# Performance work log

Hardware: AMD Instinct MI355X
Metric: run time of the kernel (lower is better)

## Reference

```python
import jax, jax.numpy as jnp
import numpy as np

INPUT_DIM = 1024
NUM_HEADS = 16
HEAD_DIM = INPUT_DIM // NUM_HEADS


def setup_inputs() -> dict:
    key = jax.random.key(0)
    ks = jax.random.split(key, 9)
    d = INPUT_DIM
    s = 1.0 / np.sqrt(d)
    x = jax.random.normal(ks[0], (2, 2048, d), dtype=jnp.float32)
    # nn.Linear default init ~ U(-1/sqrt(in), 1/sqrt(in)); weights stored as (out, in), we keep (in, out)
    Wq = jax.random.uniform(ks[1], (d, d), jnp.float32, -s, s)
    bq = jax.random.uniform(ks[2], (d,), jnp.float32, -s, s)
    Wk = jax.random.uniform(ks[3], (d, d), jnp.float32, -s, s)
    bk = jax.random.uniform(ks[4], (d,), jnp.float32, -s, s)
    Wv = jax.random.uniform(ks[5], (d, d), jnp.float32, -s, s)
    bv = jax.random.uniform(ks[6], (d,), jnp.float32, -s, s)
    Wo = jax.random.uniform(ks[7], (d, d), jnp.float32, -s, s)
    bo = jax.random.uniform(ks[8], (d,), jnp.float32, -s, s)
    return {"x": x, "Wq": Wq, "bq": bq, "Wk": Wk, "bk": bk, "Wv": Wv, "bv": bv, "Wo": Wo, "bo": bo}


def reference(x, Wq, bq, Wk, bk, Wv, bv, Wo, bo):
    b, t, d = x.shape
    h, hd = NUM_HEADS, HEAD_DIM
    # projections -> [b, h, t, hd]
    q = (x @ Wq + bq).reshape(b, t, h, hd).transpose(0, 2, 1, 3)
    k = (x @ Wk + bk).reshape(b, t, h, hd).transpose(0, 2, 1, 3)
    v = (x @ Wv + bv).reshape(b, t, h, hd).transpose(0, 2, 1, 3)
    scores = jnp.einsum('bhqd,bhkd->bhqk', q, k) / jnp.sqrt(jnp.float32(hd))
    probs = jax.nn.softmax(scores, axis=-1)
    out = jnp.einsum('bhqk,bhkd->bhqd', probs, v)
    out = out.transpose(0, 2, 1, 3).reshape(b, t, d)
    return out @ Wo + bo
```

## Files before the change

### kernel.cpp

```cpp
#include <hip/hip_runtime.h>
#include <math.h>


#define BATCH 2
#define SEQ   2048
#define DIM   1024
#define NHEAD 16
#define HDIM  64
#define MROWS (BATCH * SEQ)
#define BH    (BATCH * NHEAD)
#define NKT   (SEQ / 64)

typedef __attribute__((ext_vector_type(4))) float     floatx4;
typedef __attribute__((ext_vector_type(4))) float     float4v;
typedef __attribute__((ext_vector_type(8))) _Float16  half8;
typedef __attribute__((ext_vector_type(4))) _Float16  half4;
typedef __attribute__((ext_vector_type(2))) __fp16    fp16x2;
typedef __attribute__((ext_vector_type(4))) unsigned  uint4v;

#define SOFT_C 5.77078016f
#define QSCALE 0.18033688f

#if __has_builtin(__builtin_amdgcn_exp2f)
#define EXP2F(x) __builtin_amdgcn_exp2f(x)
#else
#define EXP2F(x) exp2f(x)
#endif

__device__ __forceinline__ void gload16(const void* g, void* l) {
    __builtin_amdgcn_global_load_lds(
        (const __attribute__((address_space(1))) unsigned int*)g,
        (__attribute__((address_space(3))) unsigned int*)l, 16, 0, 0);
}

__device__ __forceinline__ unsigned pk2(float a, float b) {
    fp16x2 v = __builtin_amdgcn_cvt_pkrtz(a, b);
    return __builtin_bit_cast(unsigned, v);
}

__device__ __forceinline__ void plswap(unsigned &a, unsigned &b) {
#if __has_builtin(__builtin_amdgcn_permlane32_swap) && __has_builtin(__builtin_amdgcn_permlane16_swap)
    auto r32 = __builtin_amdgcn_permlane32_swap(a, b, false, false);
    auto r16 = __builtin_amdgcn_permlane16_swap(r32[0], r32[1], false, false);
    a = r16[0]; b = r16[1];
#else
    asm volatile("s_nop 1\n\t"
                 "v_permlane32_swap_b32 %0, %1\n\t"
                 "s_nop 1\n\t"
                 "v_permlane16_swap_b32 %0, %1\n\t"
                 "s_nop 1"
                 : "+v"(a), "+v"(b));
#endif
}

__global__ __launch_bounds__(256) void prep(
    const float* __restrict__ x,
    const float* __restrict__ Wq, const float* __restrict__ Wk,
    const float* __restrict__ Wv, const float* __restrict__ Wo,
    _Float16* __restrict__ xh,
    _Float16* __restrict__ Wqt, _Float16* __restrict__ Wkt,
    _Float16* __restrict__ Wvt, _Float16* __restrict__ Wot)
{
    const int tid = threadIdx.x;
    if (blockIdx.z == 4) {
        const int bid = blockIdx.y * 16 + blockIdx.x;
        #pragma unroll
        for (int it = 0; it < 8; ++it) {
            const size_t i = (((size_t)it * 256 + bid) * 256 + tid) * 8;
            float4v a = *(const float4v*)(x + i);
            float4v b = *(const float4v*)(x + i + 4);
            half8 o;
            #pragma unroll
            for (int c = 0; c < 4; ++c) { o[c] = (_Float16)a[c]; o[4+c] = (_Float16)b[c]; }
            *(half8*)(xh + i) = o;
        }
        return;
    }
    __shared__ float tile[64][65];
    const float* W; _Float16* o;
    switch (blockIdx.z) {
        case 0: W = Wq; o = Wqt; break;
        case 1: W = Wk; o = Wkt; break;
        case 2: W = Wv; o = Wvt; break;
        default: W = Wo; o = Wot; break;
    }
    const int n0 = blockIdx.x * 64, k0 = blockIdx.y * 64;
    #pragma unroll
    for (int p = 0; p < 16; ++p) {
        int idx = tid + p * 256;
        int r = idx >> 6, c = idx & 63;
        tile[r][c] = W[(size_t)(k0 + r) * DIM + n0 + c];
    }
    __syncthreads();
    #pragma unroll
    for (int p = 0; p < 16; ++p) {
        int idx = tid + p * 256;
        int r = idx >> 6, c = idx & 63;
        o[(size_t)(n0 + r) * DIM + k0 + c] = (_Float16)tile[c][r];
    }
}

__device__ __forceinline__ void gemm_core32(
    const _Float16* __restrict__ Ap, const _Float16* __restrict__ Bp,
    int m0, int n0, _Float16* SH, floatx4 acc[4][4])
{
    const int tid  = threadIdx.x;
    const int wave = tid >> 6;
    const int lane = tid & 63;
    const int li   = lane & 15;
    const int quad = lane >> 4;
    const int wm   = (wave >> 1) * 64;
    const int wn   = (wave & 1) * 64;

    _Float16* AL0 = SH;
    _Float16* BL0 = SH + 4096;
    _Float16* AL1 = SH + 8192;
    _Float16* BL1 = SH + 12288;

    auto stg = [&](int k0, _Float16* AL, _Float16* BL) {
        #pragma unroll
        for (int p = 0; p < 2; ++p) {
            int s = tid + p * 256;
            int r = s >> 2, ks = s & 3;
            int kg = (ks ^ ((r >> 1) & 3)) << 3;
            int ldsb = (wave * 64 + p * 256) * 8;
            gload16(Ap + (size_t)(m0 + r) * DIM + k0 + kg, AL + ldsb);
            gload16(Bp + (size_t)(n0 + r) * DIM + k0 + kg, BL + ldsb);
        }
    };

    auto cmp = [&](const _Float16* AL, const _Float16* BL) {
        half8 a[4], b[4];
        const int cs = (quad ^ ((li >> 1) & 3)) << 3;
        #pragma unroll
        for (int i = 0; i < 4; ++i) {
            a[i] = *(const half8*)(AL + ((wm + i * 16 + li) << 5) + cs);
            b[i] = *(const half8*)(BL + ((wn + i * 16 + li) << 5) + cs);
        }
        #pragma unroll
        for (int i = 0; i < 4; ++i)
            #pragma unroll
            for (int j = 0; j < 4; ++j)
                acc[i][j] = __builtin_amdgcn_mfma_f32_16x16x32_f16(a[i], b[j], acc[i][j], 0, 0, 0);
    };

    stg(0, AL0, BL0);
    __syncthreads();

    for (int kt = 0; kt < DIM / 32; kt += 2) {
        stg((kt + 1) * 32, AL1, BL1);
        __builtin_amdgcn_s_setprio(1);
        cmp(AL0, BL0);
        __builtin_amdgcn_s_setprio(0);
        __syncthreads();
        if (kt + 2 < DIM / 32) stg((kt + 2) * 32, AL0, BL0);
        __builtin_amdgcn_s_setprio(1);
        cmp(AL1, BL1);
        __builtin_amdgcn_s_setprio(0);
        __syncthreads();
    }
}

__global__ __launch_bounds__(256, 3) void qkv_mfma(
    const _Float16* __restrict__ xh,
    const _Float16* __restrict__ Wqt, const _Float16* __restrict__ Wkt,
    const _Float16* __restrict__ Wvt,
    const float* __restrict__ bq, const float* __restrict__ bk,
    const float* __restrict__ bv,
    _Float16* __restrict__ Qh, _Float16* __restrict__ Kh,
    _Float16* __restrict__ Vth)
{
    __shared__ __align__(16) _Float16 SH[128 * 128];

    const int bid = blockIdx.x + 8 * (blockIdx.y + 32 * blockIdx.z);
    const int swz = (bid & 7) * 96 + (bid >> 3);
    const int bx  = swz & 7;
    const int by  = (swz >> 3) & 31;
    const int z   = swz >> 8;

    const _Float16* Bp; const float* bias;
    if (z == 0)      { Bp = Wqt; bias = bq; }
    else if (z == 1) { Bp = Wkt; bias = bk; }
    else             { Bp = Wvt; bias = bv; }

    const int m0 = by * 128, n0 = bx * 128;

    floatx4 acc[4][4];
    #pragma unroll
    for (int i = 0; i < 4; ++i)
        #pragma unroll
        for (int j = 0; j < 4; ++j) acc[i][j] = (floatx4){0.f, 0.f, 0.f, 0.f};

    gemm_core32(xh, Bp, m0, n0, SH, acc);

    const int tid = threadIdx.x, wave = tid >> 6, lane = tid & 63;
    const int li = lane & 15, quad = lane >> 4;
    const int wm = (wave >> 1) * 64, wn = (wave & 1) * 64;
    const int bb = m0 >> 11, t0 = m0 & 2047;

    if (z != 2) {
        _Float16* out = (z == 0) ? Qh : Kh;
        const float sc = (z == 0) ? QSCALE : 1.0f;
        #pragma unroll
        for (int i = 0; i < 4; ++i)
            #pragma unroll
            for (int j = 0; j < 4; ++j) {
                int n = n0 + wn + j * 16 + li;
                int h = n >> 6, hd = n & 63;
                float b_ = bias[n];
                #pragma unroll
                for (int r = 0; r < 4; ++r) {
                    int m = m0 + wm + i * 16 + quad * 4 + r;
                    int t = m & 2047;
                    out[(((size_t)(bb * NHEAD + h) * SEQ) + t) * HDIM + hd] =
                        (_Float16)((acc[i][j][r] + b_) * sc);
                }
            }
    } else {
        __syncthreads();
        #pragma unroll
        for (int i = 0; i < 4; ++i)
            #pragma unroll
            for (int j = 0; j < 4; ++j) {
                int n = wn + j * 16 + li;
                float b_ = bias[n0 + n];
                half4 w;
                #pragma unroll
                for (int r = 0; r < 4; ++r) w[r] = (_Float16)(acc[i][j][r] + b_);
                int col  = wm + i * 16 + quad * 4;
                int colp = ((((col >> 3) ^ (n & 7)) << 3)) | (col & 7);
                *(half4*)(SH + n * 128 + colp) = w;
            }
        __syncthreads();
        #pragma unroll
        for (int p = 0; p < 8; ++p) {
            int idx = p * 256 + tid;
            int v = idx >> 4, c8 = (idx & 15) * 8;
            int c8p = (((c8 >> 3) ^ (v & 7)) << 3);
            half8 w = *(const half8*)(SH + v * 128 + c8p);
            int n = n0 + v;
            int h = n >> 6, hd = n & 63;
            *(half8*)(Vth + ((size_t)(bb * NHEAD + h) * HDIM + hd) * SEQ + t0 + c8) = w;
        }
    }
}

__global__ __launch_bounds__(256, 2) void attn(
    const _Float16* __restrict__ Q, const _Float16* __restrict__ K,
    const _Float16* __restrict__ Vt,
    _Float16* __restrict__ Ctx)
{
    __shared__ __align__(16) _Float16 Ks[2][64 * 64];
    __shared__ __align__(16) _Float16 Vs[2][64 * 64];

    const int tid  = threadIdx.x;
    const int wave = tid >> 6;
    const int lane = tid & 63;
    const int li   = lane & 15;
    const int quad = lane >> 4;

    const int bid = blockIdx.x + 16 * blockIdx.y;
    const int swz = (bid & 7) * 64 + (bid >> 3);
    const int q0  = (swz & 15) * 128;
    const int bh  = swz >> 4;
    const int b   = bh >> 4, h = bh & 15;

    half8 qa[2][2];
    #pragma unroll
    for (int nq = 0; nq < 2; ++nq) {
        size_t qrow = ((size_t)bh * SEQ + q0 + wave * 32 + nq * 16 + li) * HDIM;
        qa[nq][0] = *(const half8*)(Q + qrow + quad * 8);
        qa[nq][1] = *(const half8*)(Q + qrow + 32 + quad * 8);
    }

    half8 onesA;
    {
        _Float16 v = (li == 0) ? (_Float16)1.0f : (_Float16)0.0f;
        #pragma unroll
        for (int c = 0; c < 8; ++c) onesA[c] = v;
    }

    floatx4 O[4][2];
    floatx4 rsacc[2];
    #pragma unroll
    for (int nq = 0; nq < 2; ++nq) {
        rsacc[nq] = (floatx4){0.f, 0.f, 0.f, 0.f};
        #pragma unroll
        for (int i = 0; i < 4; ++i) O[i][nq] = (floatx4){0.f, 0.f, 0.f, 0.f};
    }

    const _Float16* Kbh = K  + (size_t)bh * SEQ * HDIM;
    const _Float16* Vbh = Vt + (size_t)bh * HDIM * SEQ;

    auto stage = [&](int buf, int kt_) {
        const _Float16* Kg = Kbh + (size_t)kt_ * 64 * HDIM;
        const _Float16* Vg = Vbh + kt_ * 64;
        _Float16* Kl = &Ks[buf][0];
        _Float16* Vl = &Vs[buf][0];
        #pragma unroll
        for (int p = 0; p < 2; ++p) {
            int s = tid + p * 256;
            int r = s >> 3, ks = s & 7;
            int kg = (ks ^ (r & 7)) << 3;
            int ldsb = (wave * 64 + p * 256) * 8;
            gload16(Kg + r * HDIM + kg, Kl + ldsb);
            gload16(Vg + (size_t)r * SEQ + kg, Vl + ldsb);
        }
    };

    auto qk_phase = [&](const _Float16* Kc, const _Float16* Vc,
                        half8 (&pbN)[2][2], half8 (&vfN)[4][2]) {
        unsigned R[2][4][2];
        #pragma unroll
        for (int mb = 0; mb < 4; ++mb) {
            int row = (mb * 16 + li) << 6;
            half8 a0 = *(const half8*)(Kc + row + ((quad ^ (li & 7)) << 3));
            half8 a1 = *(const half8*)(Kc + row + (((quad + 4) ^ (li & 7)) << 3));
            #pragma unroll
            for (int nq = 0; nq < 2; ++nq) {
                floatx4 st = (floatx4){-SOFT_C, -SOFT_C, -SOFT_C, -SOFT_C};
                st = __builtin_amdgcn_mfma_f32_16x16x32_f16(a0, qa[nq][0], st, 0, 0, 0);
                st = __builtin_amdgcn_mfma_f32_16x16x32_f16(a1, qa[nq][1], st, 0, 0, 0);
                R[nq][mb][0] = pk2(EXP2F(st[0]), EXP2F(st[1]));
                R[nq][mb][1] = pk2(EXP2F(st[2]), EXP2F(st[3]));
            }
        }
        #pragma unroll
        for (int nq = 0; nq < 2; ++nq)
            #pragma unroll
            for (int f = 0; f < 2; ++f) {
                unsigned w0, w1, w2, w3;
                {
                    unsigned x = R[nq][2 * f][0], y = R[nq][2 * f + 1][0];
                    plswap(x, y);
                    w0 = x; w2 = y;
                }
                {
                    unsigned x = R[nq][2 * f][1], y = R[nq][2 * f + 1][1];
                    plswap(x, y);
                    w1 = x; w3 = y;
                }
                uint4v uw; uw[0] = w0; uw[1] = w1; uw[2] = w2; uw[3] = w3;
                pbN[nq][f] = __builtin_bit_cast(half8, uw);
            }
        #pragma unroll
        for (int mb = 0; mb < 4; ++mb) {
            int row = (mb * 16 + li) << 6;
            vfN[mb][0] = *(const half8*)(Vc + row + ((quad ^ (li & 7)) << 3));
            vfN[mb][1] = *(const half8*)(Vc + row + (((quad + 4) ^ (li & 7)) << 3));
        }
    };

    auto pv_phase = [&](half8 (&pbP)[2][2], half8 (&vfP)[4][2]) {
        #pragma unroll
        for (int nq = 0; nq < 2; ++nq) {
            rsacc[nq] = __builtin_amdgcn_mfma_f32_16x16x32_f16(onesA, pbP[nq][0], rsacc[nq], 0, 0, 0);
            rsacc[nq] = __builtin_amdgcn_mfma_f32_16x16x32_f16(onesA, pbP[nq][1], rsacc[nq], 0, 0, 0);
        }
        #pragma unroll
        for (int mb = 0; mb < 4; ++mb)
            #pragma unroll
            for (int nq = 0; nq < 2; ++nq) {
                O[mb][nq] = __builtin_amdgcn_mfma_f32_16x16x32_f16(vfP[mb][0], pbP[nq][0], O[mb][nq], 0, 0, 0);
                O[mb][nq] = __builtin_amdgcn_mfma_f32_16x16x32_f16(vfP[mb][1], pbP[nq][1], O[mb][nq], 0, 0, 0);
            }
    };

    half8 pbA[2][2], pbB[2][2];
    half8 vfA[4][2], vfB[4][2];

    stage(0, 0);
    __syncthreads();

    stage(1, 1);
    __builtin_amdgcn_s_setprio(1);
    qk_phase(&Ks[0][0], &Vs[0][0], pbA, vfA);
    __builtin_amdgcn_s_setprio(0);
    __syncthreads();

    for (int kt = 1; kt < NKT - 1; kt += 2) {
        stage(0, kt + 1);
        __builtin_amdgcn_s_setprio(1);
        pv_phase(pbA, vfA);
        qk_phase(&Ks[1][0], &Vs[1][0], pbB, vfB);
        __builtin_amdgcn_s_setprio(0);
        __syncthreads();

        stage(1, kt + 2);
        __builtin_amdgcn_s_setprio(1);
        pv_phase(pbB, vfB);
        qk_phase(&Ks[0][0], &Vs[0][0], pbA, vfA);
        __builtin_amdgcn_s_setprio(0);
        __syncthreads();
    }

    __builtin_amdgcn_s_setprio(1);
    pv_phase(pbA, vfA);
    qk_phase(&Ks[1][0], &Vs[1][0], pbB, vfB);
    pv_phase(pbB, vfB);
    __builtin_amdgcn_s_setprio(0);
    __syncthreads();

    float inv[2];
    #pragma unroll
    for (int nq = 0; nq < 2; ++nq) {
        float rs = __shfl(rsacc[nq][0], li, 64);
        inv[nq] = 1.0f / rs;
    }

    _Float16* Sw = &Ks[0][0] + wave * (32 * 64);
    #pragma unroll
    for (int mb = 0; mb < 4; ++mb)
        #pragma unroll
        for (int nq = 0; nq < 2; ++nq) {
            uint2 w;
            w.x = pk2(O[mb][nq][0] * inv[nq], O[mb][nq][1] * inv[nq]);
            w.y = pk2(O[mb][nq][2] * inv[nq], O[mb][nq][3] * inv[nq]);
            int row = nq * 16 + li;
            int col = mb * 16 + quad * 4;
            int swc = (((col >> 3) ^ (row & 7)) << 3) | (col & 7);
            *(uint2*)(Sw + row * 64 + swc) = w;
        }
    __builtin_amdgcn_s_waitcnt(0);
    #pragma unroll
    for (int p = 0; p < 4; ++p) {
        int idx = p * 64 + lane;
        int qq = idx >> 3, c = idx & 7;
        half8 v = *(const half8*)(Sw + qq * 64 + ((c ^ (qq & 7)) << 3));
        size_t row = (size_t)b * SEQ + q0 + wave * 32 + qq;
        *(half8*)(Ctx + row * DIM + h * HDIM + c * 8) = v;
    }
}

__global__ __launch_bounds__(256, 3) void out_mfma(
    const _Float16* __restrict__ Ctx, const _Float16* __restrict__ Wot,
    const float* __restrict__ bo, float* __restrict__ out)
{
    __shared__ __align__(16) _Float16 SH[24576];

    const int bid = blockIdx.x + 8 * blockIdx.y;
    const int swz = (bid & 7) * 64 + (bid >> 3);
    const int bx = swz & 7, by = swz >> 3;
    const int m0 = by * 64, n0 = bx * 128;

    const int tid  = threadIdx.x;
    const int wave = tid >> 6;
    const int lane = tid & 63;
    const int li   = lane & 15;
    const int quad = lane >> 4;
    const int wm   = (wave >> 1) * 32;
    const int wn   = (wave & 1) * 64;

    _Float16* A0 = SH;
    _Float16* B0 = SH + 4096;
    _Float16* A1 = SH + 12288;
    _Float16* B1 = SH + 16384;

    floatx4 acc[2][4];
    #pragma unroll
    for (int i = 0; i < 2; ++i)
        #pragma unroll
        for (int j = 0; j < 4; ++j) acc[i][j] = (floatx4){0.f, 0.f, 0.f, 0.f};

    auto stg = [&](int k0, _Float16* AL, _Float16* BL) {
        #pragma unroll
        for (int p = 0; p < 2; ++p) {
            int s = tid + p * 256;
            int r = s >> 3, ks = s & 7;
            int kg = (ks ^ (r & 7)) << 3;
            gload16(Ctx + (size_t)(m0 + r) * DIM + k0 + kg,
                    AL + (wave * 64 + p * 256) * 8);
        }
        #pragma unroll
        for (int p = 0; p < 4; ++p) {
            int s = tid + p * 256;
            int r = s >> 3, ks = s & 7;
            int kg = (ks ^ (r & 7)) << 3;
            gload16(Wot + (size_t)(n0 + r) * DIM + k0 + kg,
                    BL + (wave * 64 + p * 256) * 8);
        }
    };

    auto cmp = [&](const _Float16* AL, const _Float16* BL) {
        half8 a[2][2], b[4][2];
        #pragma unroll
        for (int i = 0; i < 2; ++i) {
            int ra = (wm + i * 16 + li) << 6;
            #pragma unroll
            for (int hh = 0; hh < 2; ++hh)
                a[i][hh] = *(const half8*)(AL + ra + (((hh * 4 + quad) ^ (li & 7)) << 3));
        }
        #pragma unroll
        for (int j = 0; j < 4; ++j) {
            int rb = (wn + j * 16 + li) << 6;
            #pragma unroll
            for (int hh = 0; hh < 2; ++hh)
                b[j][hh] = *(const half8*)(BL + rb + (((hh * 4 + quad) ^ (li & 7)) << 3));
        }
        #pragma unroll
        for (int i = 0; i < 2; ++i)
            #pragma unroll
            for (int j = 0; j < 4; ++j) {
                acc[i][j] = __builtin_amdgcn_mfma_f32_16x16x32_f16(a[i][0], b[j][0], acc[i][j], 0, 0, 0);
                acc[i][j] = __builtin_amdgcn_mfma_f32_16x16x32_f16(a[i][1], b[j][1], acc[i][j], 0, 0, 0);
            }
    };

    stg(0, A0, B0);
    __syncthreads();
    for (int kt = 0; kt < DIM / 64; kt += 2) {
        stg((kt + 1) * 64, A1, B1);
        __builtin_amdgcn_s_setprio(1);
        cmp(A0, B0);
        __builtin_amdgcn_s_setprio(0);
        __syncthreads();
        if (kt + 2 < DIM / 64) stg((kt + 2) * 64, A0, B0);
        __builtin_amdgcn_s_setprio(1);
        cmp(A1, B1);
        __builtin_amdgcn_s_setprio(0);
        __syncthreads();
    }

    #pragma unroll
    for (int i = 0; i < 2; ++i)
        #pragma unroll
        for (int j = 0; j < 4; ++j) {
            int n = n0 + wn + j * 16 + li;
            float b_ = bo[n];
            #pragma unroll
            for (int r = 0; r < 4; ++r) {
                int m = m0 + wm + i * 16 + quad * 4 + r;
                out[(size_t)m * DIM + n] = acc[i][j][r] + b_;
            }
        }
}

extern "C" void kernel_launch(void* const* d_in, const int* in_sizes, int n_in,
                              void* d_out, int out_size, void* d_ws, size_t ws_size,
                              hipStream_t stream) {
    const float* x  = (const float*)d_in[0];
    const float* Wq = (const float*)d_in[1];
    const float* bq = (const float*)d_in[2];
    const float* Wk = (const float*)d_in[3];
    const float* bk = (const float*)d_in[4];
    const float* Wv = (const float*)d_in[5];
    const float* bv = (const float*)d_in[6];
    const float* Wo = (const float*)d_in[7];
    const float* bo = (const float*)d_in[8];
    float* out = (float*)d_out;

    const size_t PX = (size_t)MROWS * DIM;
    const size_t PW = (size_t)DIM * DIM;
    _Float16* xh  = (_Float16*)d_ws;
    _Float16* Wqt = xh + PX;
    _Float16* Wkt = Wqt + PW;
    _Float16* Wvt = Wkt + PW;
    _Float16* Wot = Wvt + PW;
    _Float16* Qh  = Wot + PW;
    _Float16* Kh  = Qh + PX;
    _Float16* spare = Kh + PX;
    _Float16* Vth = spare + PX;

    _Float16* Ctx = xh;

    prep<<<dim3(16, 16, 5), 256, 0, stream>>>(
        x, Wq, Wk, Wv, Wo, xh, Wqt, Wkt, Wvt, Wot);

    qkv_mfma<<<dim3(DIM / 128, MROWS / 128, 3), 256, 0, stream>>>(
        xh, Wqt, Wkt, Wvt, bq, bk, bv, Qh, Kh, Vth);

    attn<<<dim3(SEQ / 128, BH), 256, 0, stream>>>(
        Qh, Kh, Vth, Ctx);

    out_mfma<<<dim3(8, MROWS / 64), 256, 0, stream>>>(
        Ctx, Wot, bo, out);
}
```

Baseline: 176.7 us.

## Widen attention KV tiles to 128 and triple-buffer V in shared memory

Doubles the key/value tile per iteration from 64 to 128 keys, halving the number of barrier-separated loop steps. V fragments are now read from LDS directly inside the PV phase instead of being preloaded into registers during the QK phase, and V uses a three-slot rotating buffer so the tile being consumed is not overwritten by the next stage. This cuts synchronisation and loop overhead per key but increases LDS use (about 80 KB per block), which may limit the two-blocks-per-CU occupancy and raises register pressure from the larger probability fragments.

```diff
diff --git a/kernel.cpp b/kernel.cpp
--- a/kernel.cpp
+++ b/kernel.cpp
@@ -9,7 +9,8 @@
 #define HDIM  64
 #define MROWS (BATCH * SEQ)
 #define BH    (BATCH * NHEAD)
-#define NKT   (SEQ / 64)
+#define KVB   128
+#define NKT2  (SEQ / KVB)
 
 typedef __attribute__((ext_vector_type(4))) float     floatx4;
 typedef __attribute__((ext_vector_type(4))) float     float4v;
@@ -250,8 +251,8 @@
     const _Float16* __restrict__ Vt,
     _Float16* __restrict__ Ctx)
 {
-    __shared__ __align__(16) _Float16 Ks[2][64 * 64];
-    __shared__ __align__(16) _Float16 Vs[2][64 * 64];
+    __shared__ __align__(16) _Float16 Ks[2][KVB * HDIM];
+    __shared__ __align__(16) _Float16 Vs[3][HDIM * KVB];
 
     const int tid  = threadIdx.x;
     const int wave = tid >> 6;
@@ -292,27 +293,29 @@
     const _Float16* Kbh = K  + (size_t)bh * SEQ * HDIM;
     const _Float16* Vbh = Vt + (size_t)bh * HDIM * SEQ;
 
-    auto stage = [&](int buf, int kt_) {
-        const _Float16* Kg = Kbh + (size_t)kt_ * 64 * HDIM;
-        const _Float16* Vg = Vbh + kt_ * 64;
-        _Float16* Kl = &Ks[buf][0];
-        _Float16* Vl = &Vs[buf][0];
-        #pragma unroll
-        for (int p = 0; p < 2; ++p) {
+    auto stage = [&](_Float16* Kl, _Float16* Vl, int kt_) {
+        const _Float16* Kg = Kbh + (size_t)kt_ * KVB * HDIM;
+        const _Float16* Vg = Vbh + kt_ * KVB;
+        #pragma unroll
+        for (int p = 0; p < 4; ++p) {
             int s = tid + p * 256;
             int r = s >> 3, ks = s & 7;
             int kg = (ks ^ (r & 7)) << 3;
-            int ldsb = (wave * 64 + p * 256) * 8;
-            gload16(Kg + r * HDIM + kg, Kl + ldsb);
-            gload16(Vg + (size_t)r * SEQ + kg, Vl + ldsb);
-        }
-    };
-
-    auto qk_phase = [&](const _Float16* Kc, const _Float16* Vc,
-                        half8 (&pbN)[2][2], half8 (&vfN)[4][2]) {
-        unsigned R[2][4][2];
-        #pragma unroll
-        for (int mb = 0; mb < 4; ++mb) {
+            gload16(Kg + r * HDIM + kg, Kl + s * 8);
+        }
+        #pragma unroll
+        for (int p = 0; p < 4; ++p) {
+            int s = tid + p * 256;
+            int r = s >> 4, ks = s & 15;
+            int kg = (ks ^ (r & 15)) << 3;
+            gload16(Vg + (size_t)r * SEQ + kg, Vl + s * 8);
+        }
+    };
+
+    auto qk_phase = [&](const _Float16* Kc, half8 (&pbN)[2][4]) {
+        unsigned R[2][8][2];
+        #pragma unroll
+        for (int mb = 0; mb < 8; ++mb) {
             int row = (mb * 16 + li) << 6;
             half8 a0 = *(const half8*)(Kc + row + ((quad ^ (li & 7)) << 3));
             half8 a1 = *(const half8*)(Kc + row + (((quad + 4) ^ (li & 7)) << 3));
@@ -328,76 +331,79 @@
         #pragma unroll
         for (int nq = 0; nq < 2; ++nq)
             #pragma unroll
-            for (int f = 0; f < 2; ++f) {
+            for (int kc = 0; kc < 4; ++kc) {
                 unsigned w0, w1, w2, w3;
                 {
-                    unsigned x = R[nq][2 * f][0], y = R[nq][2 * f + 1][0];
+                    unsigned x = R[nq][2 * kc][0], y = R[nq][2 * kc + 1][0];
                     plswap(x, y);
                     w0 = x; w2 = y;
                 }
                 {
-                    unsigned x = R[nq][2 * f][1], y = R[nq][2 * f + 1][1];
+                    unsigned x = R[nq][2 * kc][1], y = R[nq][2 * kc + 1][1];
                     plswap(x, y);
                     w1 = x; w3 = y;
                 }
                 uint4v uw; uw[0] = w0; uw[1] = w1; uw[2] = w2; uw[3] = w3;
-                pbN[nq][f] = __builtin_bit_cast(half8, uw);
-            }
+                pbN[nq][kc] = __builtin_bit_cast(half8, uw);
+            }
+    };
+
+    auto pv_phase = [&](half8 (&pbP)[2][4], const _Float16* Vc) {
+        #pragma unroll
+        for (int nq = 0; nq < 2; ++nq)
+            #pragma unroll
+            for (int kc = 0; kc < 4; ++kc)
+                rsacc[nq] = __builtin_amdgcn_mfma_f32_16x16x32_f16(onesA, pbP[nq][kc], rsacc[nq], 0, 0, 0);
         #pragma unroll
         for (int mb = 0; mb < 4; ++mb) {
-            int row = (mb * 16 + li) << 6;
-            vfN[mb][0] = *(const half8*)(Vc + row + ((quad ^ (li & 7)) << 3));
-            vfN[mb][1] = *(const half8*)(Vc + row + (((quad + 4) ^ (li & 7)) << 3));
-        }
-    };
-
-    auto pv_phase = [&](half8 (&pbP)[2][2], half8 (&vfP)[4][2]) {
-        #pragma unroll
-        for (int nq = 0; nq < 2; ++nq) {
-            rsacc[nq] = __builtin_amdgcn_mfma_f32_16x16x32_f16(onesA, pbP[nq][0], rsacc[nq], 0, 0, 0);
-            rsacc[nq] = __builtin_amdgcn_mfma_f32_16x16x32_f16(onesA, pbP[nq][1], rsacc[nq], 0, 0, 0);
-        }
-        #pragma unroll
-        for (int mb = 0; mb < 4; ++mb)
-            #pragma unroll
-            for (int nq = 0; nq < 2; ++nq) {
-                O[mb][nq] = __builtin_amdgcn_mfma_f32_16x16x32_f16(vfP[mb][0], pbP[nq][0], O[mb][nq], 0, 0, 0);
-                O[mb][nq] = __builtin_amdgcn_mfma_f32_16x16x32_f16(vfP[mb][1], pbP[nq][1], O[mb][nq], 0, 0, 0);
-            }
-    };
-
-    half8 pbA[2][2], pbB[2][2];
-    half8 vfA[4][2], vfB[4][2];
-
-    stage(0, 0);
+            int rowb = (mb * 16 + li) * KVB;
+            #pragma unroll
+            for (int kc = 0; kc < 4; ++kc) {
+                half8 vf = *(const half8*)(Vc + rowb + ((((kc * 4 + quad) ^ li)) << 3));
+                #pragma unroll
+                for (int nq = 0; nq < 2; ++nq)
+                    O[mb][nq] = __builtin_amdgcn_mfma_f32_16x16x32_f16(vf, pbP[nq][kc], O[mb][nq], 0, 0, 0);
+            }
+        }
+    };
+
+    half8 pbA[2][4], pbB[2][4];
+
+    stage(&Ks[0][0], &Vs[0][0], 0);
     __syncthreads();
 
-    stage(1, 1);
+    stage(&Ks[1][0], &Vs[1][0], 1);
     __builtin_amdgcn_s_setprio(1);
-    qk_phase(&Ks[0][0], &Vs[0][0], pbA, vfA);
+    qk_phase(&Ks[0][0], pbA);
     __builtin_amdgcn_s_setprio(0);
     __syncthreads();
 
-    for (int kt = 1; kt < NKT - 1; kt += 2) {
-        stage(0, kt + 1);
+    _Float16* va = &Vs[0][0];
+    _Float16* vb = &Vs[1][0];
+    _Float16* vc = &Vs[2][0];
+
+    for (int kt = 1; kt < NKT2 - 1; kt += 2) {
+        stage(&Ks[0][0], vc, kt + 1);
         __builtin_amdgcn_s_setprio(1);
-        pv_phase(pbA, vfA);
-        qk_phase(&Ks[1][0], &Vs[1][0], pbB, vfB);
+        pv_phase(pbA, va);
+        qk_phase(&Ks[1][0], pbB);
         __builtin_amdgcn_s_setprio(0);
         __syncthreads();
-
-        stage(1, kt + 2);
+        { _Float16* t = va; va = vb; vb = vc; vc = t; }
+
+        stage(&Ks[1][0], vc, kt + 2);
         __builtin_amdgcn_s_setprio(1);
-        pv_phase(pbB, vfB);
-        qk_phase(&Ks[0][0], &Vs[0][0], pbA, vfA);
+        pv_phase(pbB, va);
+        qk_phase(&Ks[0][0], pbA);
         __builtin_amdgcn_s_setprio(0);
         __syncthreads();
+        { _Float16* t = va; va = vb; vb = vc; vc = t; }
     }
 
     __builtin_amdgcn_s_setprio(1);
-    pv_phase(pbA, vfA);
-    qk_phase(&Ks[1][0], &Vs[1][0], pbB, vfB);
-    pv_phase(pbB, vfB);
+    pv_phase(pbA, va);
+    qk_phase(&Ks[1][0], pbB);
+    pv_phase(pbB, vb);
     __builtin_amdgcn_s_setprio(0);
     __syncthreads();
 
```

Result: no change. 173.8 us, median of 2 (-1.7%).

## Shrink attention query tile to 64 rows to raise occupancy and grid size

Applied to the files above, without the earlier changes.

The attention kernel now handles 64 query rows per block instead of 128, with each wave covering 16 query rows rather than 32. This halves per-thread accumulator and score registers, so launch bounds can request 4 blocks per SM, and it doubles the grid to 1024 blocks. The trade-off is that every K/V tile is loaded from global memory into LDS twice as often per query row, and each wave gets less MFMA work per LDS fragment read.

```diff
diff --git a/kernel.cpp b/kernel.cpp
--- a/kernel.cpp
+++ b/kernel.cpp
@@ -245,7 +245,7 @@
     }
 }
 
-__global__ __launch_bounds__(256, 2) void attn(
+__global__ __launch_bounds__(256, 4) void attn(
     const _Float16* __restrict__ Q, const _Float16* __restrict__ K,
     const _Float16* __restrict__ Vt,
     _Float16* __restrict__ Ctx)
@@ -259,18 +259,18 @@
     const int li   = lane & 15;
     const int quad = lane >> 4;
 
-    const int bid = blockIdx.x + 16 * blockIdx.y;
-    const int swz = (bid & 7) * 64 + (bid >> 3);
-    const int q0  = (swz & 15) * 128;
-    const int bh  = swz >> 4;
+    const int bid = blockIdx.x + 32 * blockIdx.y;
+    const int swz = (bid & 7) * 128 + (bid >> 3);
+    const int q0  = (swz & 31) * 64;
+    const int bh  = swz >> 5;
     const int b   = bh >> 4, h = bh & 15;
-
-    half8 qa[2][2];
-    #pragma unroll
-    for (int nq = 0; nq < 2; ++nq) {
-        size_t qrow = ((size_t)bh * SEQ + q0 + wave * 32 + nq * 16 + li) * HDIM;
-        qa[nq][0] = *(const half8*)(Q + qrow + quad * 8);
-        qa[nq][1] = *(const half8*)(Q + qrow + 32 + quad * 8);
+    const int wq  = wave * 16;
+
+    half8 qa0, qa1;
+    {
+        size_t qrow = ((size_t)bh * SEQ + q0 + wq + li) * HDIM;
+        qa0 = *(const half8*)(Q + qrow + quad * 8);
+        qa1 = *(const half8*)(Q + qrow + 32 + quad * 8);
     }
 
     half8 onesA;
@@ -280,14 +280,10 @@
         for (int c = 0; c < 8; ++c) onesA[c] = v;
     }
 
-    floatx4 O[4][2];
-    floatx4 rsacc[2];
-    #pragma unroll
-    for (int nq = 0; nq < 2; ++nq) {
-        rsacc[nq] = (floatx4){0.f, 0.f, 0.f, 0.f};
-        #pragma unroll
-        for (int i = 0; i < 4; ++i) O[i][nq] = (floatx4){0.f, 0.f, 0.f, 0.f};
-    }
+    floatx4 O[4];
+    floatx4 rsacc = (floatx4){0.f, 0.f, 0.f, 0.f};
+    #pragma unroll
+    for (int i = 0; i < 4; ++i) O[i] = (floatx4){0.f, 0.f, 0.f, 0.f};
 
     const _Float16* Kbh = K  + (size_t)bh * SEQ * HDIM;
     const _Float16* Vbh = Vt + (size_t)bh * HDIM * SEQ;
@@ -309,40 +305,35 @@
     };
 
     auto qk_phase = [&](const _Float16* Kc, const _Float16* Vc,
-                        half8 (&pbN)[2][2], half8 (&vfN)[4][2]) {
-        unsigned R[2][4][2];
+                        half8 (&pbN)[2], half8 (&vfN)[4][2]) {
+        unsigned R[4][2];
         #pragma unroll
         for (int mb = 0; mb < 4; ++mb) {
             int row = (mb * 16 + li) << 6;
             half8 a0 = *(const half8*)(Kc + row + ((quad ^ (li & 7)) << 3));
             half8 a1 = *(const half8*)(Kc + row + (((quad + 4) ^ (li & 7)) << 3));
-            #pragma unroll
-            for (int nq = 0; nq < 2; ++nq) {
-                floatx4 st = (floatx4){-SOFT_C, -SOFT_C, -SOFT_C, -SOFT_C};
-                st = __builtin_amdgcn_mfma_f32_16x16x32_f16(a0, qa[nq][0], st, 0, 0, 0);
-                st = __builtin_amdgcn_mfma_f32_16x16x32_f16(a1, qa[nq][1], st, 0, 0, 0);
-                R[nq][mb][0] = pk2(EXP2F(st[0]), EXP2F(st[1]));
-                R[nq][mb][1] = pk2(EXP2F(st[2]), EXP2F(st[3]));
+            floatx4 st = (floatx4){-SOFT_C, -SOFT_C, -SOFT_C, -SOFT_C};
+            st = __builtin_amdgcn_mfma_f32_16x16x32_f16(a0, qa0, st, 0, 0, 0);
+            st = __builtin_amdgcn_mfma_f32_16x16x32_f16(a1, qa1, st, 0, 0, 0);
+            R[mb][0] = pk2(EXP2F(st[0]), EXP2F(st[1]));
+            R[mb][1] = pk2(EXP2F(st[2]), EXP2F(st[3]));
+        }
+        #pragma unroll
+        for (int f = 0; f < 2; ++f) {
+            unsigned w0, w1, w2, w3;
+            {
+                unsigned x = R[2 * f][0], y = R[2 * f + 1][0];
+                plswap(x, y);
+                w0 = x; w2 = y;
             }
-        }
-        #pragma unroll
-        for (int nq = 0; nq < 2; ++nq)
-            #pragma unroll
-            for (int f = 0; f < 2; ++f) {
-                unsigned w0, w1, w2, w3;
-                {
-                    unsigned x = R[nq][2 * f][0], y = R[nq][2 * f + 1][0];
-                    plswap(x, y);
-                    w0 = x; w2 = y;
-                }
-                {
-                    unsigned x = R[nq][2 * f][1], y = R[nq][2 * f + 1][1];
-                    plswap(x, y);
-                    w1 = x; w3 = y;
-                }
-                uint4v uw; uw[0] = w0; uw[1] = w1; uw[2] = w2; uw[3] = w3;
-                pbN[nq][f] = __builtin_bit_cast(half8, uw);
+            {
+                unsigned x = R[2 * f][1], y = R[2 * f + 1][1];
+                plswap(x, y);
+                w1 = x; w3 = y;
             }
+            uint4v uw; uw[0] = w0; uw[1] = w1; uw[2] = w2; uw[3] = w3;
+            pbN[f] = __builtin_bit_cast(half8, uw);
+        }
         #pragma unroll
         for (int mb = 0; mb < 4; ++mb) {
             int row = (mb * 16 + li) << 6;
@@ -351,22 +342,17 @@
         }
     };
 
-    auto pv_phase = [&](half8 (&pbP)[2][2], half8 (&vfP)[4][2]) {
-        #pragma unroll
-        for (int nq = 0; nq < 2; ++nq) {
-            rsacc[nq] = __builtin_amdgcn_mfma_f32_16x16x32_f16(onesA, pbP[nq][0], rsacc[nq], 0, 0, 0);
-            rsacc[nq] = __builtin_amdgcn_mfma_f32_16x16x32_f16(onesA, pbP[nq][1], rsacc[nq], 0, 0, 0);
-        }
-        #pragma unroll
-        for (int mb = 0; mb < 4; ++mb)
-            #pragma unroll
-            for (int nq = 0; nq < 2; ++nq) {
-                O[mb][nq] = __builtin_amdgcn_mfma_f32_16x16x32_f16(vfP[mb][0], pbP[nq][0], O[mb][nq], 0, 0, 0);
-                O[mb][nq] = __builtin_amdgcn_mfma_f32_16x16x32_f16(vfP[mb][1], pbP[nq][1], O[mb][nq], 0, 0, 0);
-            }
-    };
-
-    half8 pbA[2][2], pbB[2][2];
+    auto pv_phase = [&](half8 (&pbP)[2], half8 (&vfP)[4][2]) {
+        rsacc = __builtin_amdgcn_mfma_f32_16x16x32_f16(onesA, pbP[0], rsacc, 0, 0, 0);
+        rsacc = __builtin_amdgcn_mfma_f32_16x16x32_f16(onesA, pbP[1], rsacc, 0, 0, 0);
+        #pragma unroll
+        for (int mb = 0; mb < 4; ++mb) {
+            O[mb] = __builtin_amdgcn_mfma_f32_16x16x32_f16(vfP[mb][0], pbP[0], O[mb], 0, 0, 0);
+            O[mb] = __builtin_amdgcn_mfma_f32_16x16x32_f16(vfP[mb][1], pbP[1], O[mb], 0, 0, 0);
+        }
+    };
+
+    half8 pbA[2], pbB[2];
     half8 vfA[4][2], vfB[4][2];
 
     stage(0, 0);
@@ -401,33 +387,26 @@
     __builtin_amdgcn_s_setprio(0);
     __syncthreads();
 
-    float inv[2];
-    #pragma unroll
-    for (int nq = 0; nq < 2; ++nq) {
-        float rs = __shfl(rsacc[nq][0], li, 64);
-        inv[nq] = 1.0f / rs;
-    }
-
-    _Float16* Sw = &Ks[0][0] + wave * (32 * 64);
-    #pragma unroll
-    for (int mb = 0; mb < 4; ++mb)
-        #pragma unroll
-        for (int nq = 0; nq < 2; ++nq) {
-            uint2 w;
-            w.x = pk2(O[mb][nq][0] * inv[nq], O[mb][nq][1] * inv[nq]);
-            w.y = pk2(O[mb][nq][2] * inv[nq], O[mb][nq][3] * inv[nq]);
-            int row = nq * 16 + li;
-            int col = mb * 16 + quad * 4;
-            int swc = (((col >> 3) ^ (row & 7)) << 3) | (col & 7);
-            *(uint2*)(Sw + row * 64 + swc) = w;
-        }
+    const float inv = 1.0f / __shfl(rsacc[0], li, 64);
+
+    _Float16* Sw = &Ks[0][0] + wave * (16 * 64);
+    #pragma unroll
+    for (int mb = 0; mb < 4; ++mb) {
+        uint2 w;
+        w.x = pk2(O[mb][0] * inv, O[mb][1] * inv);
+        w.y = pk2(O[mb][2] * inv, O[mb][3] * inv);
+        int row = li;
+        int col = mb * 16 + quad * 4;
+        int swc = (((col >> 3) ^ (row & 7)) << 3) | (col & 7);
+        *(uint2*)(Sw + row * 64 + swc) = w;
+    }
     __builtin_amdgcn_s_waitcnt(0);
     #pragma unroll
-    for (int p = 0; p < 4; ++p) {
+    for (int p = 0; p < 2; ++p) {
         int idx = p * 64 + lane;
         int qq = idx >> 3, c = idx & 7;
         half8 v = *(const half8*)(Sw + qq * 64 + ((c ^ (qq & 7)) << 3));
-        size_t row = (size_t)b * SEQ + q0 + wave * 32 + qq;
+        size_t row = (size_t)b * SEQ + q0 + wq + qq;
         *(half8*)(Ctx + row * DIM + h * HDIM + c * 8) = v;
     }
 }
@@ -569,7 +548,7 @@
     qkv_mfma<<<dim3(DIM / 128, MROWS / 128, 3), 256, 0, stream>>>(
         xh, Wqt, Wkt, Wvt, bq, bk, bv, Qh, Kh, Vth);
 
-    attn<<<dim3(SEQ / 128, BH), 256, 0, stream>>>(
+    attn<<<dim3(SEQ / 64, BH), 256, 0, stream>>>(
         Qh, Kh, Vth, Ctx);
 
     out_mfma<<<dim3(8, MROWS / 64), 256, 0, stream>>>(
```

Result: slower. 184.3 us (+4.3%).
